# Performance work log

Measured on AMD Instinct MI355X. Metric: run time of the kernel, lower is better.

## Reference

```python
import jax, jax.numpy as jnp
import numpy as np

N_NODES = 10000
N_EDGES = 640000
N_GRAPHS = 64
IN_FEAT = 128
HID = (128, 128)
NUM_CLASS = 10


def setup_inputs() -> dict:
    key = jax.random.key(0)
    ks = jax.random.split(key, 10)
    x = jax.random.normal(ks[0], (N_NODES, IN_FEAT), dtype=jnp.float32)
    edge_index = jax.random.randint(ks[1], (2, N_EDGES), 0, N_NODES, dtype=jnp.int64)
    batch = jnp.sort(jax.random.randint(ks[2], (N_NODES,), 0, N_GRAPHS, dtype=jnp.int64))
    # GCNConv weights (PyG applies x @ W then propagates, bias added after aggregation)
    s1 = 1.0 / np.sqrt(IN_FEAT)
    s2 = 1.0 / np.sqrt(HID[0])
    s3 = 1.0 / np.sqrt(HID[1])
    W1 = jax.random.uniform(ks[3], (IN_FEAT, HID[0]), jnp.float32, -s1, s1)
    b1 = jnp.zeros((HID[0],), jnp.float32)
    W2 = jax.random.uniform(ks[4], (HID[0], HID[1]), jnp.float32, -s2, s2)
    b2 = jnp.zeros((HID[1],), jnp.float32)
    Wlin = jax.random.uniform(ks[5], (HID[1], NUM_CLASS), jnp.float32, -s3, s3)
    blin = jax.random.uniform(ks[6], (NUM_CLASS,), jnp.float32, -s3, s3)
    return {"x": x, "edge_index": edge_index, "batch": batch,
            "W1": W1, "b1": b1, "W2": W2, "b2": b2, "Wlin": Wlin, "blin": blin}


def _gcn_conv(x, src, dst, W, b):
    # GCNConv with self-loops and symmetric normalization:
    # out[i] = sum_{(j->i) in E} d[j]^{-1/2} d[i]^{-1/2} (x_j W) + d[i]^{-1} (x_i W) + b
    # where d = in-degree (on dst) + 1 for the self-loop.
    h = x @ W                                                      # [N, F]
    ones = jnp.ones(src.shape[0], dtype=h.dtype)
    deg = jax.ops.segment_sum(ones, dst, num_segments=x.shape[0]) + 1.0
    dinv = jax.lax.rsqrt(deg)                                      # [N]
    norm = dinv[src] * dinv[dst]                                   # [E]
    agg = jax.ops.segment_sum(h[src] * norm[:, None], dst, num_segments=x.shape[0])
    agg = agg + h * (dinv * dinv)[:, None]                         # self-loop term
    return agg + b


def _global_mean_pool(x, batch, num_graphs):
    sums = jax.ops.segment_sum(x, batch, num_segments=num_graphs)          # [G, F]
    cnt = jax.ops.segment_sum(jnp.ones(x.shape[0], x.dtype), batch, num_segments=num_graphs)
    return sums / jnp.maximum(cnt, 1.0)[:, None]


def reference(x, edge_index, batch, W1, b1, W2, b2, Wlin, blin):
    src, dst = edge_index[0], edge_index[1]
    h = jax.nn.relu(_gcn_conv(x, src, dst, W1, b1))
    h = jax.nn.relu(_gcn_conv(h, src, dst, W2, b2))
    g = _global_mean_pool(h, batch, N_GRAPHS)      # [G, hid1]
    return g @ Wlin + blin                          # [G, num_class]
```

## Files before the change

kernel.cpp:

```cpp
#include <hip/hip_runtime.h>
#include <hip/hip_bf16.h>

#define NN 10000
#define NE 640000
#define NG 64
#define NF 128
#define NC 10
#define TM 32
#define TKC 32
#define NB 250
#define BSZ 40
#define G1 512
#define ECHUNK 1250


__device__ __forceinline__ unsigned short f2bf(float f) {
    unsigned int u = __float_as_uint(f);
    return (unsigned short)((u + 0x7FFF + ((u >> 16) & 1)) >> 16);
}
__device__ __forceinline__ float bf_lo(unsigned int p) {
    return __uint_as_float(p << 16);
}
__device__ __forceinline__ float bf_hi(unsigned int p) {
    return __uint_as_float(p & 0xFFFF0000u);
}

__device__ __forceinline__ int detect64(const int* w, long span) {
    int lane = threadIdx.x & 63;
    long e = (long)lane * (span - 1) / 63;
    return (__ballot(w[2 * e + 1] != 0) == 0ULL) ? 1 : 0;
}

__device__ __forceinline__ int ld_idx(const void* p, long i, int is64) {
    return is64 ? (int)((const long long*)p)[i] : ((const int*)p)[i];
}

__global__ __launch_bounds__(256) void k_hist(const void* __restrict__ ei,
                                              int* __restrict__ bh) {
    int is64 = detect64((const int*)ei, NE);
    __shared__ int hist[256];
    int tid = threadIdx.x;
    hist[tid] = 0;
    __syncthreads();
    int e0 = blockIdx.x * ECHUNK, e1 = min(NE, e0 + ECHUNK);
    for (int e = e0 + tid; e < e1; e += 256) {
        int dst = ld_idx(ei, (long)NE + e, is64);
        atomicAdd(&hist[dst / BSZ], 1);
    }
    __syncthreads();
    bh[tid * G1 + blockIdx.x] = hist[tid];
}

__global__ __launch_bounds__(256) void k_bscan1(int* __restrict__ bh,
                                                int* __restrict__ btot) {
    int w = blockIdx.x * 4 + (threadIdx.x >> 6);
    if (w >= NB) return;
    int lane = threadIdx.x & 63;
    int base = w * G1 + lane * 8;
    int vals[8];
    int lsum = 0;
#pragma unroll
    for (int i = 0; i < 8; ++i) { vals[i] = bh[base + i]; lsum += vals[i]; }
    int pref = lsum;
    for (int o = 1; o < 64; o <<= 1) {
        int t = __shfl_up(pref, o, 64);
        if (lane >= o) pref += t;
    }
    int run = pref - lsum;
#pragma unroll
    for (int i = 0; i < 8; ++i) { int v = vals[i]; bh[base + i] = run; run += v; }
    if (lane == 63) btot[w] = run;
}

__global__ __launch_bounds__(256) void k_bscan2(const int* __restrict__ btot,
                                                int* __restrict__ bbase) {
    __shared__ int s[256];
    int tid = threadIdx.x;
    s[tid] = (tid < NB) ? btot[tid] : 0;
    __syncthreads();
    if (tid == 0) {
        int run = 0;
        for (int b = 0; b < NB; ++b) { int v = s[b]; s[b] = run; run += v; }
    }
    __syncthreads();
    if (tid < NB) bbase[tid] = s[tid];
    if (tid == 0) bbase[NB] = NE;
}

__global__ __launch_bounds__(256) void k_bucket(const void* __restrict__ ei,
                                                const int* __restrict__ bh,
                                                const int* __restrict__ bbase,
                                                int* __restrict__ ebuf) {
    int is64 = detect64((const int*)ei, NE);
    __shared__ int cur[256];
    int tid = threadIdx.x;
    if (tid < NB) cur[tid] = bh[tid * G1 + blockIdx.x] + bbase[tid];
    __syncthreads();
    int e0 = blockIdx.x * ECHUNK, e1 = min(NE, e0 + ECHUNK);
    for (int e = e0 + tid; e < e1; e += 256) {
        int dst = ld_idx(ei, (long)NE + e, is64);
        int src = ld_idx(ei, (long)e, is64);
        int b = dst / BSZ;
        int p = atomicAdd(&cur[b], 1);
        ebuf[p] = ((dst - b * BSZ) << 14) | src;
    }
}

__global__ __launch_bounds__(256) void k_csr(const int* __restrict__ ebuf,
                                             const int* __restrict__ bbase,
                                             int* __restrict__ coff,
                                             float* __restrict__ dinv,
                                             int* __restrict__ csrc) {
    __shared__ int dcount[BSZ];
    __shared__ int dstart[BSZ];
    __shared__ int cur[BSZ];
    int b = blockIdx.x, tid = threadIdx.x;
    if (tid < BSZ) dcount[tid] = 0;
    __syncthreads();
    int base = bbase[b], end = bbase[b + 1];
    for (int i = base + tid; i < end; i += 256)
        atomicAdd(&dcount[ebuf[i] >> 14], 1);
    __syncthreads();
    if (tid == 0) {
        int run = 0;
        for (int i = 0; i < BSZ; ++i) {
            dstart[i] = run; cur[i] = base + run; run += dcount[i];
        }
    }
    __syncthreads();
    if (tid < BSZ) {
        coff[b * BSZ + tid] = base + dstart[tid];
        dinv[b * BSZ + tid] = rsqrtf((float)dcount[tid] + 1.0f);
    }
    if (b == NB - 1 && tid == 0) coff[NN] = NE;
    __syncthreads();
    for (int i = base + tid; i < end; i += 256) {
        int pk = ebuf[i];
        int p = atomicAdd(&cur[pk >> 14], 1);
        csrc[p] = pk & 16383;
    }
}

__global__ __launch_bounds__(256) void k_gemm(const float* __restrict__ X,
                                              const float* __restrict__ W,
                                              const float* __restrict__ dinv,
                                              unsigned short* __restrict__ Y,
                                              int nrows) {
    __shared__ float sX[TKC * 36];
    __shared__ float sW[32 * 132];
    int tid = threadIdx.x;
    int rg = tid & 7;
    int cg = tid >> 3;
    int m0 = blockIdx.x * TM;
    float acc[4][4] = {{0.f}};
    for (int kc = 0; kc < NF / TKC; ++kc) {
        int k0 = kc * TKC;
        {
            int row = tid >> 3, kq = tid & 7;
            int mm = m0 + row; if (mm > nrows - 1) mm = nrows - 1;
            float4 v = *(const float4*)(X + (size_t)mm * NF + k0 + kq * 4);
            sX[(kq * 4 + 0) * 36 + row] = v.x;
            sX[(kq * 4 + 1) * 36 + row] = v.y;
            sX[(kq * 4 + 2) * 36 + row] = v.z;
            sX[(kq * 4 + 3) * 36 + row] = v.w;
        }
#pragma unroll
        for (int j = 0; j < 4; ++j) {
            int idx = tid + 256 * j;
            int k = idx >> 5, cq = idx & 31;
            float4 v = *(const float4*)(W + (size_t)(k0 + k) * NF + cq * 4);
            *(float4*)(sW + cq * 132 + k * 4) = v;
        }
        __syncthreads();
#pragma unroll 8
        for (int k = 0; k < TKC; ++k) {
            float4 xf = *(const float4*)(sX + k * 36 + rg * 4);
            float4 wf = *(const float4*)(sW + cg * 132 + k * 4);
            acc[0][0] = fmaf(xf.x, wf.x, acc[0][0]);
            acc[0][1] = fmaf(xf.x, wf.y, acc[0][1]);
            acc[0][2] = fmaf(xf.x, wf.z, acc[0][2]);
            acc[0][3] = fmaf(xf.x, wf.w, acc[0][3]);
            acc[1][0] = fmaf(xf.y, wf.x, acc[1][0]);
            acc[1][1] = fmaf(xf.y, wf.y, acc[1][1]);
            acc[1][2] = fmaf(xf.y, wf.z, acc[1][2]);
            acc[1][3] = fmaf(xf.y, wf.w, acc[1][3]);
            acc[2][0] = fmaf(xf.z, wf.x, acc[2][0]);
            acc[2][1] = fmaf(xf.z, wf.y, acc[2][1]);
            acc[2][2] = fmaf(xf.z, wf.z, acc[2][2]);
            acc[2][3] = fmaf(xf.z, wf.w, acc[2][3]);
            acc[3][0] = fmaf(xf.w, wf.x, acc[3][0]);
            acc[3][1] = fmaf(xf.w, wf.y, acc[3][1]);
            acc[3][2] = fmaf(xf.w, wf.z, acc[3][2]);
            acc[3][3] = fmaf(xf.w, wf.w, acc[3][3]);
        }
        __syncthreads();
    }
#pragma unroll
    for (int r = 0; r < 4; ++r) {
        int m = m0 + rg * 4 + r;
        if (m < nrows) {
            float ds = dinv[m];
            ushort4 h;
            h.x = f2bf(acc[r][0] * ds);
            h.y = f2bf(acc[r][1] * ds);
            h.z = f2bf(acc[r][2] * ds);
            h.w = f2bf(acc[r][3] * ds);
            *(ushort4*)(Y + (size_t)m * NF + cg * 4) = h;
        }
    }
}

__global__ __launch_bounds__(256) void k_gather(const unsigned short* __restrict__ G,
                                                const int* __restrict__ off,
                                                const int* __restrict__ csrc,
                                                const float* __restrict__ dinv,
                                                const float* __restrict__ bias,
                                                float* __restrict__ OUT) {
    int wid = threadIdx.x >> 6, lane = threadIdx.x & 63;
    int half = lane >> 5;
    int c4 = lane & 31;
    int n = blockIdx.x * 4 + wid;
    if (n >= NN) return;
    int beg = off[n], end = off[n + 1];
    float din = dinv[n];
    float4 acc = make_float4(0.f, 0.f, 0.f, 0.f);
    int e = beg + half;
    for (; e + 6 < end; e += 8) {
        int s0 = csrc[e];
        int s1 = csrc[e + 2];
        int s2 = csrc[e + 4];
        int s3 = csrc[e + 6];
        uint2 p0 = ((const uint2*)(G + (size_t)s0 * NF))[c4];
        uint2 p1 = ((const uint2*)(G + (size_t)s1 * NF))[c4];
        uint2 p2 = ((const uint2*)(G + (size_t)s2 * NF))[c4];
        uint2 p3 = ((const uint2*)(G + (size_t)s3 * NF))[c4];
        acc.x += bf_lo(p0.x); acc.y += bf_hi(p0.x);
        acc.z += bf_lo(p0.y); acc.w += bf_hi(p0.y);
        acc.x += bf_lo(p1.x); acc.y += bf_hi(p1.x);
        acc.z += bf_lo(p1.y); acc.w += bf_hi(p1.y);
        acc.x += bf_lo(p2.x); acc.y += bf_hi(p2.x);
        acc.z += bf_lo(p2.y); acc.w += bf_hi(p2.y);
        acc.x += bf_lo(p3.x); acc.y += bf_hi(p3.x);
        acc.z += bf_lo(p3.y); acc.w += bf_hi(p3.y);
    }
    for (; e < end; e += 2) {
        int s = csrc[e];
        uint2 p = ((const uint2*)(G + (size_t)s * NF))[c4];
        acc.x += bf_lo(p.x); acc.y += bf_hi(p.x);
        acc.z += bf_lo(p.y); acc.w += bf_hi(p.y);
    }
    acc.x += __shfl_xor(acc.x, 32);
    acc.y += __shfl_xor(acc.y, 32);
    acc.z += __shfl_xor(acc.z, 32);
    acc.w += __shfl_xor(acc.w, 32);
    if (half == 0) {
        uint2 sp = ((const uint2*)(G + (size_t)n * NF))[c4];
        float4 bb = ((const float4*)bias)[c4];
        float4 o;
        o.x = fmaxf(fmaf(din, acc.x + bf_lo(sp.x), bb.x), 0.f);
        o.y = fmaxf(fmaf(din, acc.y + bf_hi(sp.x), bb.y), 0.f);
        o.z = fmaxf(fmaf(din, acc.z + bf_lo(sp.y), bb.z), 0.f);
        o.w = fmaxf(fmaf(din, acc.w + bf_hi(sp.y), bb.w), 0.f);
        ((float4*)(OUT + (size_t)n * NF))[c4] = o;
    }
}

__global__ __launch_bounds__(256) void k_poolfin(const float* __restrict__ H,
                                                 const void* __restrict__ batch,
                                                 const float* __restrict__ Wl,
                                                 const float* __restrict__ bl,
                                                 float* __restrict__ out) {
    int is64 = detect64((const int*)batch, NN / 2);
    __shared__ int sb[2];
    __shared__ float4 part[256];
    __shared__ float pooled[NF];
    int g = blockIdx.x;
    int tid = threadIdx.x;
    if (tid < 2) {
        int target = g + tid;
        int lo = 0, hi = NN;
        while (lo < hi) {
            int mid = (lo + hi) >> 1;
            if (ld_idx(batch, mid, is64) < target) lo = mid + 1; else hi = mid;
        }
        sb[tid] = lo;
    }
    __syncthreads();
    int beg = sb[0], end = sb[1];
    int c4 = tid & 31, r = tid >> 5;
    float4 acc = make_float4(0.f, 0.f, 0.f, 0.f);
    for (int n = beg + r; n < end; n += 8) {
        float4 v = ((const float4*)(H + (size_t)n * NF))[c4];
        acc.x += v.x; acc.y += v.y; acc.z += v.z; acc.w += v.w;
    }
    part[tid] = acc;
    __syncthreads();
    if (tid < 32) {
        float4 s = part[tid];
#pragma unroll
        for (int j = 1; j < 8; j++) {
            float4 p = part[tid + 32 * j];
            s.x += p.x; s.y += p.y; s.z += p.z; s.w += p.w;
        }
        float ic = 1.0f / fmaxf((float)(end - beg), 1.0f);
        pooled[tid * 4 + 0] = s.x * ic;
        pooled[tid * 4 + 1] = s.y * ic;
        pooled[tid * 4 + 2] = s.z * ic;
        pooled[tid * 4 + 3] = s.w * ic;
    }
    __syncthreads();
    if (tid < NC) {
        float a = bl[tid];
#pragma unroll 8
        for (int k = 0; k < NF; k++)
            a = fmaf(pooled[k], Wl[k * NC + tid], a);
        out[g * NC + tid] = a;
    }
}

extern "C" void kernel_launch(void* const* d_in, const int* in_sizes, int n_in,
                              void* d_out, int out_size, void* d_ws, size_t ws_size,
                              hipStream_t stream) {
    const float* x  = (const float*)d_in[0];
    const void*  ei = d_in[1];
    const void*  bt = d_in[2];
    const float* W1 = (const float*)d_in[3];
    const float* b1 = (const float*)d_in[4];
    const float* W2 = (const float*)d_in[5];
    const float* b2 = (const float*)d_in[6];
    const float* Wl = (const float*)d_in[7];
    const float* bl = (const float*)d_in[8];

    char* ws = (char*)d_ws;
    int*   coff  = (int*)(ws + 0);
    int*   bbase = (int*)(ws + 40016);
    int*   btot  = (int*)(ws + 41040);
    float* dinv  = (float*)(ws + 42064);
    int*   csrc  = (int*)(ws + 82064);
    unsigned short* Gb = (unsigned short*)(ws + 2642064);
    float* bufB  = (float*)(ws + 7762064);
    int*   bh    = (int*)(ws + 2642064);
    int*   ebuf  = (int*)(ws + 7762064);

    k_hist  <<<G1, 256, 0, stream>>>(ei, bh);
    k_bscan1<<<(NB + 3) / 4, 256, 0, stream>>>(bh, btot);
    k_bscan2<<<1, 256, 0, stream>>>(btot, bbase);
    k_bucket<<<G1, 256, 0, stream>>>(ei, bh, bbase, ebuf);
    k_csr   <<<NB, 256, 0, stream>>>(ebuf, bbase, coff, dinv, csrc);

    k_gemm<<<(NN + TM - 1) / TM, 256, 0, stream>>>(x, W1, dinv, Gb, NN);
    k_gather<<<(NN + 3) / 4, 256, 0, stream>>>(Gb, coff, csrc, dinv, b1, bufB);
    k_gemm<<<(NN + TM - 1) / TM, 256, 0, stream>>>(bufB, W2, dinv, Gb, NN);
    k_gather<<<(NN + 3) / 4, 256, 0, stream>>>(Gb, coff, csrc, dinv, b2, bufB);

    k_poolfin<<<NG, 256, 0, stream>>>(bufB, bt, Wl, bl, (float*)d_out);
}
```

Measured before the change: 175.7 us.

## Store CSR sources as 16-bit and gather 16-byte rows with four edge lanes

```diff
diff --git a/kernel.cpp b/kernel.cpp
--- a/kernel.cpp
+++ b/kernel.cpp
@@ -110,7 +110,7 @@
                                              const int* __restrict__ bbase,
                                              int* __restrict__ coff,
                                              float* __restrict__ dinv,
-                                             int* __restrict__ csrc) {
+                                             unsigned short* __restrict__ csrc) {
     __shared__ int dcount[BSZ];
     __shared__ int dstart[BSZ];
     __shared__ int cur[BSZ];
@@ -137,7 +137,7 @@
     for (int i = base + tid; i < end; i += 256) {
         int pk = ebuf[i];
         int p = atomicAdd(&cur[pk >> 14], 1);
-        csrc[p] = pk & 16383;
+        csrc[p] = (unsigned short)(pk & 16383);
     }
 }
 
@@ -212,56 +212,66 @@
 
 __global__ __launch_bounds__(256) void k_gather(const unsigned short* __restrict__ G,
                                                 const int* __restrict__ off,
-                                                const int* __restrict__ csrc,
+                                                const unsigned short* __restrict__ csrc,
                                                 const float* __restrict__ dinv,
                                                 const float* __restrict__ bias,
                                                 float* __restrict__ OUT) {
     int wid = threadIdx.x >> 6, lane = threadIdx.x & 63;
-    int half = lane >> 5;
-    int c4 = lane & 31;
+    int q = lane >> 4, f = lane & 15;
     int n = blockIdx.x * 4 + wid;
     if (n >= NN) return;
     int beg = off[n], end = off[n + 1];
     float din = dinv[n];
-    float4 acc = make_float4(0.f, 0.f, 0.f, 0.f);
-    int e = beg + half;
-    for (; e + 6 < end; e += 8) {
+    float a0 = 0.f, a1 = 0.f, a2 = 0.f, a3 = 0.f;
+    float a4 = 0.f, a5 = 0.f, a6 = 0.f, a7 = 0.f;
+    int e = beg + q;
+    for (; e + 12 < end; e += 16) {
         int s0 = csrc[e];
-        int s1 = csrc[e + 2];
-        int s2 = csrc[e + 4];
-        int s3 = csrc[e + 6];
-        uint2 p0 = ((const uint2*)(G + (size_t)s0 * NF))[c4];
-        uint2 p1 = ((const uint2*)(G + (size_t)s1 * NF))[c4];
-        uint2 p2 = ((const uint2*)(G + (size_t)s2 * NF))[c4];
-        uint2 p3 = ((const uint2*)(G + (size_t)s3 * NF))[c4];
-        acc.x += bf_lo(p0.x); acc.y += bf_hi(p0.x);
-        acc.z += bf_lo(p0.y); acc.w += bf_hi(p0.y);
-        acc.x += bf_lo(p1.x); acc.y += bf_hi(p1.x);
-        acc.z += bf_lo(p1.y); acc.w += bf_hi(p1.y);
-        acc.x += bf_lo(p2.x); acc.y += bf_hi(p2.x);
-        acc.z += bf_lo(p2.y); acc.w += bf_hi(p2.y);
-        acc.x += bf_lo(p3.x); acc.y += bf_hi(p3.x);
-        acc.z += bf_lo(p3.y); acc.w += bf_hi(p3.y);
-    }
-    for (; e < end; e += 2) {
+        int s1 = csrc[e + 4];
+        int s2 = csrc[e + 8];
+        int s3 = csrc[e + 12];
+        uint4 p0 = ((const uint4*)(G + (size_t)s0 * NF))[f];
+        uint4 p1 = ((const uint4*)(G + (size_t)s1 * NF))[f];
+        uint4 p2 = ((const uint4*)(G + (size_t)s2 * NF))[f];
+        uint4 p3 = ((const uint4*)(G + (size_t)s3 * NF))[f];
+        a0 += bf_lo(p0.x); a1 += bf_hi(p0.x); a2 += bf_lo(p0.y); a3 += bf_hi(p0.y);
+        a4 += bf_lo(p0.z); a5 += bf_hi(p0.z); a6 += bf_lo(p0.w); a7 += bf_hi(p0.w);
+        a0 += bf_lo(p1.x); a1 += bf_hi(p1.x); a2 += bf_lo(p1.y); a3 += bf_hi(p1.y);
+        a4 += bf_lo(p1.z); a5 += bf_hi(p1.z); a6 += bf_lo(p1.w); a7 += bf_hi(p1.w);
+        a0 += bf_lo(p2.x); a1 += bf_hi(p2.x); a2 += bf_lo(p2.y); a3 += bf_hi(p2.y);
+        a4 += bf_lo(p2.z); a5 += bf_hi(p2.z); a6 += bf_lo(p2.w); a7 += bf_hi(p2.w);
+        a0 += bf_lo(p3.x); a1 += bf_hi(p3.x); a2 += bf_lo(p3.y); a3 += bf_hi(p3.y);
+        a4 += bf_lo(p3.z); a5 += bf_hi(p3.z); a6 += bf_lo(p3.w); a7 += bf_hi(p3.w);
+    }
+    for (; e < end; e += 4) {
         int s = csrc[e];
-        uint2 p = ((const uint2*)(G + (size_t)s * NF))[c4];
-        acc.x += bf_lo(p.x); acc.y += bf_hi(p.x);
-        acc.z += bf_lo(p.y); acc.w += bf_hi(p.y);
-    }
-    acc.x += __shfl_xor(acc.x, 32);
-    acc.y += __shfl_xor(acc.y, 32);
-    acc.z += __shfl_xor(acc.z, 32);
-    acc.w += __shfl_xor(acc.w, 32);
-    if (half == 0) {
-        uint2 sp = ((const uint2*)(G + (size_t)n * NF))[c4];
-        float4 bb = ((const float4*)bias)[c4];
-        float4 o;
-        o.x = fmaxf(fmaf(din, acc.x + bf_lo(sp.x), bb.x), 0.f);
-        o.y = fmaxf(fmaf(din, acc.y + bf_hi(sp.x), bb.y), 0.f);
-        o.z = fmaxf(fmaf(din, acc.z + bf_lo(sp.y), bb.z), 0.f);
-        o.w = fmaxf(fmaf(din, acc.w + bf_hi(sp.y), bb.w), 0.f);
-        ((float4*)(OUT + (size_t)n * NF))[c4] = o;
+        uint4 p = ((const uint4*)(G + (size_t)s * NF))[f];
+        a0 += bf_lo(p.x); a1 += bf_hi(p.x); a2 += bf_lo(p.y); a3 += bf_hi(p.y);
+        a4 += bf_lo(p.z); a5 += bf_hi(p.z); a6 += bf_lo(p.w); a7 += bf_hi(p.w);
+    }
+    a0 += __shfl_xor(a0, 16); a1 += __shfl_xor(a1, 16);
+    a2 += __shfl_xor(a2, 16); a3 += __shfl_xor(a3, 16);
+    a4 += __shfl_xor(a4, 16); a5 += __shfl_xor(a5, 16);
+    a6 += __shfl_xor(a6, 16); a7 += __shfl_xor(a7, 16);
+    a0 += __shfl_xor(a0, 32); a1 += __shfl_xor(a1, 32);
+    a2 += __shfl_xor(a2, 32); a3 += __shfl_xor(a3, 32);
+    a4 += __shfl_xor(a4, 32); a5 += __shfl_xor(a5, 32);
+    a6 += __shfl_xor(a6, 32); a7 += __shfl_xor(a7, 32);
+    if (q == 0) {
+        uint4 sp = ((const uint4*)(G + (size_t)n * NF))[f];
+        float4 b0 = ((const float4*)bias)[2 * f];
+        float4 b1 = ((const float4*)bias)[2 * f + 1];
+        float4 o0, o1;
+        o0.x = fmaxf(fmaf(din, a0 + bf_lo(sp.x), b0.x), 0.f);
+        o0.y = fmaxf(fmaf(din, a1 + bf_hi(sp.x), b0.y), 0.f);
+        o0.z = fmaxf(fmaf(din, a2 + bf_lo(sp.y), b0.z), 0.f);
+        o0.w = fmaxf(fmaf(din, a3 + bf_hi(sp.y), b0.w), 0.f);
+        o1.x = fmaxf(fmaf(din, a4 + bf_lo(sp.z), b1.x), 0.f);
+        o1.y = fmaxf(fmaf(din, a5 + bf_hi(sp.z), b1.y), 0.f);
+        o1.z = fmaxf(fmaf(din, a6 + bf_lo(sp.w), b1.z), 0.f);
+        o1.w = fmaxf(fmaf(din, a7 + bf_hi(sp.w), b1.w), 0.f);
+        ((float4*)(OUT + (size_t)n * NF))[2 * f] = o0;
+        ((float4*)(OUT + (size_t)n * NF))[2 * f + 1] = o1;
     }
 }
 
@@ -332,15 +342,15 @@
     const float* bl = (const float*)d_in[8];
 
     char* ws = (char*)d_ws;
-    int*   coff  = (int*)(ws + 0);
-    int*   bbase = (int*)(ws + 40016);
-    int*   btot  = (int*)(ws + 41040);
-    float* dinv  = (float*)(ws + 42064);
-    int*   csrc  = (int*)(ws + 82064);
-    unsigned short* Gb = (unsigned short*)(ws + 2642064);
-    float* bufB  = (float*)(ws + 7762064);
-    int*   bh    = (int*)(ws + 2642064);
-    int*   ebuf  = (int*)(ws + 7762064);
+    int*            coff  = (int*)(ws + 0);
+    int*            bbase = (int*)(ws + 40016);
+    int*            btot  = (int*)(ws + 41040);
+    float*          dinv  = (float*)(ws + 42064);
+    unsigned short* csrc  = (unsigned short*)(ws + 82064);
+    unsigned short* Gb    = (unsigned short*)(ws + 1362064);
+    float*          bufB  = (float*)(ws + 3922064);
+    int*            bh    = (int*)(ws + 1362064);
+    int*            ebuf  = (int*)(ws + 3922064);
 
     k_hist  <<<G1, 256, 0, stream>>>(ei, bh);
     k_bscan1<<<(NB + 3) / 4, 256, 0, stream>>>(bh, btot);
```

After: 166.8 us. -5.1%, faster.
